# Kernel tuning notes

Measured on AMD Instinct MI355X. Metric: run time of the kernel, lower is better.

## Reference

```python
import jax, jax.numpy as jnp
import numpy as np

H = 51      # lstm_out, hard-coded in the module
L = 3       # num_lstms
IN = 2      # input_dim = f_in(1) + f_time(1)
B = 1024
T = 2048


def _softplus(x):
    # log(1+exp(x)) with the module's inf guard (softplus==inf -> x),
    # written in a grad-safe clipped form (identical in fp32 range).
    x_safe = jnp.minimum(x, 30.0)
    return jnp.where(x > 30.0, x, jnp.log1p(jnp.exp(x_safe)))


def setup_inputs() -> dict:
    key = jax.random.key(0)
    ks = jax.random.split(key, 2 + 4 * L + 2)
    inp = {}
    inp["input"] = jax.random.normal(ks[0], (B, T, 1), dtype=jnp.float32)
    inp["time_idx"] = jax.random.normal(ks[1], (B, T, 1), dtype=jnp.float32)
    k = 1.0 / np.sqrt(H)  # PyTorch LSTMCell/Linear default init scale
    idx = 2
    for l in range(L):
        d_in = IN if l == 0 else H
        inp[f"W_ih{l}"] = jax.random.uniform(ks[idx], (4 * H, d_in), jnp.float32, -k, k); idx += 1
        inp[f"W_hh{l}"] = jax.random.uniform(ks[idx], (4 * H, H), jnp.float32, -k, k); idx += 1
        inp[f"b_ih{l}"] = jax.random.uniform(ks[idx], (4 * H,), jnp.float32, -k, k); idx += 1
        inp[f"b_hh{l}"] = jax.random.uniform(ks[idx], (4 * H,), jnp.float32, -k, k); idx += 1
    inp["W_lin"] = jax.random.uniform(ks[idx], (2, H), jnp.float32, -k, k); idx += 1
    inp["b_lin"] = jax.random.uniform(ks[idx], (2,), jnp.float32, -k, k)
    inp["future"] = 0
    return inp


def _cell(x_t, h, c, W_ih, W_hh, b_ih, b_hh):
    # PyTorch LSTMCell: gates in order i, f, g, o
    gates = x_t @ W_ih.T + b_ih + h @ W_hh.T + b_hh  # (B, 4H)
    i, f, g, o = jnp.split(gates, 4, axis=-1)
    c_new = jax.nn.sigmoid(f) * c + jax.nn.sigmoid(i) * jnp.tanh(g)
    h_new = jax.nn.sigmoid(o) * jnp.tanh(c_new)
    return h_new, c_new


def reference(input, time_idx,
              W_ih0, W_hh0, b_ih0, b_hh0,
              W_ih1, W_hh1, b_ih1, b_hh1,
              W_ih2, W_hh2, b_ih2, b_hh2,
              W_lin, b_lin, future):
    params = [(W_ih0, W_hh0, b_ih0, b_hh0),
              (W_ih1, W_hh1, b_ih1, b_hh1),
              (W_ih2, W_hh2, b_ih2, b_hh2)]
    bsz = input.shape[0]
    # future == 0: time_idx covers exactly the conditioning context
    x = jnp.concatenate([input, time_idx], axis=2)  # (B, T, IN)
    xs = jnp.swapaxes(x, 0, 1)                       # (T, B, IN)
    h0 = jnp.zeros((L, bsz, H), dtype=input.dtype)
    c0 = jnp.zeros((L, bsz, H), dtype=input.dtype)

    def step(carry, x_t):
        hs, cs = carry
        inp_l = x_t
        nh, nc = [], []
        for l, (Wih, Whh, bih, bhh) in enumerate(params):
            h_new, c_new = _cell(inp_l, hs[l], cs[l], Wih, Whh, bih, bhh)
            nh.append(h_new); nc.append(c_new)
            inp_l = h_new
        out = inp_l @ W_lin.T + b_lin  # (B, 2) from linear1
        return (jnp.stack(nh), jnp.stack(nc)), out

    _, outs = jax.lax.scan(step, (h0, c0), xs)  # (T, B, 2)
    outs = jnp.swapaxes(outs, 0, 1)             # (B, T, 2)
    mean = outs[..., 0]
    std = _softplus(outs[..., 1])               # positivity constraint on col 1
    return jnp.stack([mean, std], axis=-1)
```

## Files before the change

kernel.cpp:

```cpp
#include <hip/hip_runtime.h>
#include <cstddef>
#include <cstdint>

#define Hd 51
#define Td 2048
#define NBb 4
#define NTH 768
#define NBLK 256

typedef _Float16 f16x8 __attribute__((ext_vector_type(8)));
typedef _Float16 f16x4 __attribute__((ext_vector_type(4)));
typedef float    f32x4 __attribute__((ext_vector_type(4)));

#define RB0   128
#define RB12  256
#define BASE0 0
#define BASE1 4096
#define BASE2 12288
#define PRE   20480
#define XP    32768
#define LDSB  65536

#define LOG2E  1.44269504f
#define LOG2E2 2.88539008f

__device__ __forceinline__ int vaddr(int base, int rowB, int db, int n, int off) {
    return base + db * (16 * rowB) + ((off >> 4) << 8) + (n << 4) + (off & 15);
}

__device__ __forceinline__ int pslot(int m4, int n) {
    return ((m4 ^ n) & 15) | (n << 4);
}

__device__ __forceinline__ float fast_rcp(float x) { return __builtin_amdgcn_rcpf(x); }
__device__ __forceinline__ float exp2_fast(float x) {
#if __has_builtin(__builtin_amdgcn_exp2f)
    return __builtin_amdgcn_exp2f(x);
#else
    return exp2f(x);
#endif
}

__device__ __forceinline__ float sigm2(float ap)  { return fast_rcp(1.f + exp2_fast(-ap)); }
__device__ __forceinline__ float tanh2(float ap)  { return fmaf(2.f, fast_rcp(1.f + exp2_fast(-ap)), -1.f); }
__device__ __forceinline__ float tanh_c(float x) {
    float e = exp2_fast(-LOG2E2 * fabsf(x));
    float t = (1.f - e) * fast_rcp(1.f + e);
    return copysignf(t, x);
}

__global__ __launch_bounds__(NTH, 3)
void lstm3_mfma(const float* __restrict__ g_input, const float* __restrict__ g_time,
                const float* __restrict__ Wih0, const float* __restrict__ Whh0,
                const float* __restrict__ bih0, const float* __restrict__ bhh0,
                const float* __restrict__ Wih1, const float* __restrict__ Whh1,
                const float* __restrict__ bih1, const float* __restrict__ bhh1,
                const float* __restrict__ Wih2, const float* __restrict__ Whh2,
                const float* __restrict__ bih2, const float* __restrict__ bhh2,
                const float* __restrict__ Wlin, const float* __restrict__ blin,
                float* __restrict__ g_out)
{
    __shared__ __align__(16) unsigned char lds[LDSB];

    const int tid  = threadIdx.x;
    const int lane = tid & 63;
    const int w    = tid >> 6;
    const int g    = w >> 2;
    const int c    = w & 3;
    const int ncol = lane & 15;
    const int kg   = lane >> 4;
    const int b0   = blockIdx.x * NBb;

    for (int i = tid * 4; i < LDSB; i += NTH * 4) *(uint32_t*)(lds + i) = 0u;
    __syncthreads();

    if (tid < 32) {
        int db = tid >> 4, n = tid & 15;
        *(unsigned short*)(lds + vaddr(BASE0, RB0,  db, n,  54 * 2)) = 0x3C00;
        *(unsigned short*)(lds + vaddr(BASE1, RB12, db, n, 112 * 2)) = 0x3C00;
        *(unsigned short*)(lds + vaddr(BASE2, RB12, db, n, 112 * 2)) = 0x3C00;
    } else if (tid >= 64 && tid < 72) {
        int i = tid - 64; int n = i & 3, f = i >> 2;
        const float* src = f ? g_time : g_input;
        float v = src[(size_t)(b0 + n) * Td];
        *(_Float16*)(lds + vaddr(BASE0, RB0, 0, n, (52 + f) * 2)) = (_Float16)v;
    }

    for (int i = tid; i < 4096; i += NTH) {
        const int f  = i >> 11;
        const int rm = i & 2047;
        const int n  = rm >> 9;
        const int t4 = rm & 511;
        const float* src = f ? g_time : g_input;
        float4 v = *(const float4*)&src[(size_t)(b0 + n) * Td + 4 * t4];
        const int slot = f * 4 + n;
        #pragma unroll
        for (int j = 0; j < 4; ++j)
            *(_Float16*)(lds + XP + ((((4 * t4 + j) << 3) + slot) << 1)) = (_Float16)((&v.x)[j]);
    }

    const int er = 16 * c + ncol;
    const bool rvalid = (er < Hd);
    f16x8 AF[16];

    if (g == 0) {
        #pragma unroll
        for (int gs = 0; gs < 4; ++gs) {
            const int sr = gs * Hd + er;
            const float S = (gs == 2) ? LOG2E2 : LOG2E;
            #pragma unroll
            for (int s = 0; s < 2; ++s)
                #pragma unroll
                for (int e = 0; e < 8; ++e) {
                    const int kk = 32 * s + 8 * kg + e;
                    float v = 0.f;
                    if (rvalid) {
                        if (kk < 51)                   v = Whh0[sr * 51 + kk];
                        else if (kk == 52 || kk == 53) v = Wih0[sr * 2 + (kk - 52)];
                        else if (kk == 54)             v = bih0[sr] + bhh0[sr];
                    }
                    AF[gs * 2 + s][e] = (_Float16)(v * S);
                }
        }
    } else {
        const float* Wih = (g == 1) ? Wih1 : Wih2;
        const float* Whh = (g == 1) ? Whh1 : Whh2;
        const float* bihp = (g == 1) ? bih1 : bih2;
        const float* bhhp = (g == 1) ? bhh1 : bhh2;
        #pragma unroll
        for (int gs = 0; gs < 4; ++gs) {
            const int sr = gs * Hd + er;
            const float S = (gs == 2) ? LOG2E2 : LOG2E;
            #pragma unroll
            for (int s = 0; s < 4; ++s)
                #pragma unroll
                for (int e = 0; e < 8; ++e) {
                    const int kk = 32 * s + 8 * kg + e;
                    float v = 0.f;
                    float sc = S;
                    if (rvalid) {
                        if (kk < 51)                   v = Wih[sr * 51 + kk];
                        else if (kk >= 56 && kk < 107) v = Whh[sr * 51 + (kk - 56)];
                        else if (kk == 112)            v = bihp[sr] + bhhp[sr];
                    } else if (g == 2 && gs == 0 && (er == 52 || er == 53)) {
                        const int hr = er - 52;
                        sc = 1.f;
                        if (kk >= 56 && kk < 107)      v = Wlin[hr * 51 + (kk - 56)];
                        else if (kk == 112)            v = blin[hr];
                    }
                    AF[gs * 4 + s][e] = (_Float16)(v * sc);
                }
        }
    }

    const f32x4 Z = {0.f, 0.f, 0.f, 0.f};
    const int PAR0 = 16 * RB0;
    const int PAR12 = 16 * RB12;
    int rd0a = vaddr(BASE0, RB0, 0, ncol, 16 * kg);
    int rd0b = vaddr(BASE0, RB0, 0, ncol, 64 + 16 * kg);
    int rd12[4];
    {
        const int baseg = (g == 2) ? BASE2 : BASE1;
        #pragma unroll
        for (int s = 0; s < 4; ++s) rd12[s] = vaddr(baseg, RB12, 0, ncol, 64 * s + 16 * kg);
    }
    const int e0 = 16 * c + 4 * kg;
    int pw[4];
    bool pwok[4];
    #pragma unroll
    for (int r = 0; r < 4; ++r) {
        pw[r] = PRE + ((g * 4 + c) << 10) + (pslot(4 * kg + r, ncol & 3) << 4);
        pwok[r] = (ncol < 4) && (e0 + r < Hd);
    }

    const bool uok = (lane < 51);
    int prd = 0, wh1 = 0, wh2 = 0, str1 = 0;
    bool has2 = false;
    if (uok) {
        const int u  = w * 51 + lane;
        const int rr = u - g * 204;
        const int ue = rr >> 2;
        const int un = rr & 3;
        prd = PRE + ((g * 4 + (ue >> 4)) << 10) + (pslot(ue & 15, un) << 4);
        if (g == 0) {
            wh1 = vaddr(BASE0, RB0,  0, un, 2 * ue);       str1 = PAR0;
            wh2 = vaddr(BASE1, RB12, 0, un, 2 * ue);       has2 = true;
        } else if (g == 1) {
            wh1 = vaddr(BASE1, RB12, 0, un, 112 + 2 * ue); str1 = PAR12;
            wh2 = vaddr(BASE2, RB12, 0, un, 2 * ue);       has2 = true;
        } else {
            wh1 = vaddr(BASE2, RB12, 0, un, 112 + 2 * ue); str1 = PAR12;
        }
    }
    float ucs = 0.f;

    f16x8 zf;
    #pragma unroll
    for (int e = 0; e < 8; ++e) zf[e] = (_Float16)0.f;
    f16x8 B0 = zf, B1 = zf;
    f16x8 Bv0 = zf, Bv1 = zf, Bv2 = zf, Bv3 = zf;

    __syncthreads();

    for (int n = 0; n <= Td + 2; ++n) {
        const int rb = n & 1, wb = rb ^ 1;
        const int rP0 = rb * PAR0, rP12 = rb * PAR12;

        if (g == 0) {
            const bool dopf = (w == 0 && lane < 8 && (n + 1) < Td);
            _Float16 pfh = (_Float16)0.f;
            const int nb = lane & 3, f = lane >> 2;
            if (dopf)
                pfh = *(const _Float16*)(lds + XP + ((((n + 1) << 3) + lane) << 1));
            if (n < Td) {
                if (ncol < 4) {
                    B0 = *(const f16x8*)(lds + rd0a + rP0);
                    B1 = *(const f16x8*)(lds + rd0b + rP0);
                }
                f32x4 a_i = Z, a_f = Z, a_g = Z, a_o = Z;
                __builtin_amdgcn_s_setprio(1);
                a_i = __builtin_amdgcn_mfma_f32_16x16x32_f16(AF[0], B0, a_i, 0, 0, 0);
                a_i = __builtin_amdgcn_mfma_f32_16x16x32_f16(AF[1], B1, a_i, 0, 0, 0);
                a_f = __builtin_amdgcn_mfma_f32_16x16x32_f16(AF[2], B0, a_f, 0, 0, 0);
                a_f = __builtin_amdgcn_mfma_f32_16x16x32_f16(AF[3], B1, a_f, 0, 0, 0);
                a_g = __builtin_amdgcn_mfma_f32_16x16x32_f16(AF[4], B0, a_g, 0, 0, 0);
                a_g = __builtin_amdgcn_mfma_f32_16x16x32_f16(AF[5], B1, a_g, 0, 0, 0);
                a_o = __builtin_amdgcn_mfma_f32_16x16x32_f16(AF[6], B0, a_o, 0, 0, 0);
                a_o = __builtin_amdgcn_mfma_f32_16x16x32_f16(AF[7], B1, a_o, 0, 0, 0);
                __builtin_amdgcn_s_setprio(0);
                #pragma unroll
                for (int r = 0; r < 4; ++r)
                    if (pwok[r]) {
                        f32x4 v = {a_i[r], a_f[r], a_g[r], a_o[r]};
                        *(f32x4*)(lds + pw[r]) = v;
                    }
            }
            if (dopf)
                *(_Float16*)(lds + vaddr(BASE0, RB0, wb, nb, (52 + f) * 2)) = pfh;
        } else {
            const bool act = (g == 1) ? (n >= 1 && n <= Td) : (n >= 2);
            if (act) {
                if (ncol < 4) {
                    Bv0 = *(const f16x8*)(lds + rd12[0] + rP12);
                    Bv1 = *(const f16x8*)(lds + rd12[1] + rP12);
                    Bv2 = *(const f16x8*)(lds + rd12[2] + rP12);
                    Bv3 = *(const f16x8*)(lds + rd12[3] + rP12);
                }
                f32x4 a_i = Z, a_f = Z, a_g = Z, a_o = Z;
                __builtin_amdgcn_s_setprio(1);
                a_i = __builtin_amdgcn_mfma_f32_16x16x32_f16(AF[0],  Bv0, a_i, 0, 0, 0);
                a_f = __builtin_amdgcn_mfma_f32_16x16x32_f16(AF[4],  Bv0, a_f, 0, 0, 0);
                a_g = __builtin_amdgcn_mfma_f32_16x16x32_f16(AF[8],  Bv0, a_g, 0, 0, 0);
                a_o = __builtin_amdgcn_mfma_f32_16x16x32_f16(AF[12], Bv0, a_o, 0, 0, 0);
                a_i = __builtin_amdgcn_mfma_f32_16x16x32_f16(AF[1],  Bv1, a_i, 0, 0, 0);
                a_f = __builtin_amdgcn_mfma_f32_16x16x32_f16(AF[5],  Bv1, a_f, 0, 0, 0);
                a_g = __builtin_amdgcn_mfma_f32_16x16x32_f16(AF[9],  Bv1, a_g, 0, 0, 0);
                a_o = __builtin_amdgcn_mfma_f32_16x16x32_f16(AF[13], Bv1, a_o, 0, 0, 0);
                a_i = __builtin_amdgcn_mfma_f32_16x16x32_f16(AF[2],  Bv2, a_i, 0, 0, 0);
                a_f = __builtin_amdgcn_mfma_f32_16x16x32_f16(AF[6],  Bv2, a_f, 0, 0, 0);
                a_g = __builtin_amdgcn_mfma_f32_16x16x32_f16(AF[10], Bv2, a_g, 0, 0, 0);
                a_o = __builtin_amdgcn_mfma_f32_16x16x32_f16(AF[14], Bv2, a_o, 0, 0, 0);
                a_i = __builtin_amdgcn_mfma_f32_16x16x32_f16(AF[3],  Bv3, a_i, 0, 0, 0);
                a_f = __builtin_amdgcn_mfma_f32_16x16x32_f16(AF[7],  Bv3, a_f, 0, 0, 0);
                a_g = __builtin_amdgcn_mfma_f32_16x16x32_f16(AF[11], Bv3, a_g, 0, 0, 0);
                a_o = __builtin_amdgcn_mfma_f32_16x16x32_f16(AF[15], Bv3, a_o, 0, 0, 0);
                __builtin_amdgcn_s_setprio(0);
                #pragma unroll
                for (int r = 0; r < 4; ++r)
                    if (pwok[r]) {
                        f32x4 v = {a_i[r], a_f[r], a_g[r], a_o[r]};
                        *(f32x4*)(lds + pw[r]) = v;
                    }
                if (g == 2 && w == 11 && kg == 1 && ncol < 4 && n >= 3) {
                    float mean = a_i[0];
                    float spre = a_i[1];
                    float sp = (spre > 30.f) ? spre : __logf(1.f + __expf(spre));
                    const int t = n - 3;
                    float2 o2 = make_float2(mean, sp);
                    *(float2*)&g_out[((size_t)(b0 + ncol) * Td + t) * 2] = o2;
                }
            }
        }
        __syncthreads();

        if (uok) {
            const int t_u = n - g;
            if (t_u >= 0 && t_u < Td) {
                f32x4 v = *(const f32x4*)(lds + prd);
                float si = sigm2(v[0]);
                float sf = sigm2(v[1]);
                float gg = tanh2(v[2]);
                float go = sigm2(v[3]);
                float cn = fmaf(sf, ucs, si * gg);
                ucs = cn;
                _Float16 hf = (_Float16)(go * tanh_c(cn));
                *(_Float16*)(lds + wh1 + wb * str1) = hf;
                if (has2) *(_Float16*)(lds + wh2 + wb * PAR12) = hf;
            }
        }
        __syncthreads();
    }
}

extern "C" void kernel_launch(void* const* d_in, const int* in_sizes, int n_in,
                              void* d_out, int out_size, void* d_ws, size_t ws_size,
                              hipStream_t stream) {
    const float* input = (const float*)d_in[0];
    const float* timei = (const float*)d_in[1];
    const float* Wih0  = (const float*)d_in[2];
    const float* Whh0  = (const float*)d_in[3];
    const float* bih0  = (const float*)d_in[4];
    const float* bhh0  = (const float*)d_in[5];
    const float* Wih1  = (const float*)d_in[6];
    const float* Whh1  = (const float*)d_in[7];
    const float* bih1  = (const float*)d_in[8];
    const float* bhh1  = (const float*)d_in[9];
    const float* Wih2  = (const float*)d_in[10];
    const float* Whh2  = (const float*)d_in[11];
    const float* bih2  = (const float*)d_in[12];
    const float* bhh2  = (const float*)d_in[13];
    const float* Wlin  = (const float*)d_in[14];
    const float* blin  = (const float*)d_in[15];
    float* out = (float*)d_out;

    lstm3_mfma<<<dim3(NBLK), dim3(NTH), 0, stream>>>(
        input, timei,
        Wih0, Whh0, bih0, bhh0,
        Wih1, Whh1, bih1, bhh1,
        Wih2, Whh2, bih2, bhh2,
        Wlin, blin, out);
}
```

Baseline: 1.985 ms.

## Fuse gate activation into MFMA waves and drop mid-step barrier

Each wave now applies the LSTM cell update to the gate pre-activations it just wrote to LDS, so the update is done by the same wave (mapped by lane to element/batch) instead of a separate pass after a block-wide barrier. This removes one __syncthreads per timestep of the 2051-step recurrence. The output head is also moved into the update path, reading the linear-head results from LDS. It relies on each wave only reading gate values it wrote itself, enforced with an lgkmcnt wait and a scheduling barrier, which is a correctness risk if the slot mapping is wrong.

```diff
diff --git a/kernel.cpp b/kernel.cpp
--- a/kernel.cpp
+++ b/kernel.cpp
@@ -165,32 +165,29 @@
         for (int s = 0; s < 4; ++s) rd12[s] = vaddr(baseg, RB12, 0, ncol, 64 * s + 16 * kg);
     }
     const int e0 = 16 * c + 4 * kg;
+    const int elim = (g == 2) ? 54 : Hd;
     int pw[4];
     bool pwok[4];
     #pragma unroll
     for (int r = 0; r < 4; ++r) {
         pw[r] = PRE + ((g * 4 + c) << 10) + (pslot(4 * kg + r, ncol & 3) << 4);
-        pwok[r] = (ncol < 4) && (e0 + r < Hd);
-    }
-
-    const bool uok = (lane < 51);
-    int prd = 0, wh1 = 0, wh2 = 0, str1 = 0;
-    bool has2 = false;
-    if (uok) {
-        const int u  = w * 51 + lane;
-        const int rr = u - g * 204;
-        const int ue = rr >> 2;
-        const int un = rr & 3;
-        prd = PRE + ((g * 4 + (ue >> 4)) << 10) + (pslot(ue & 15, un) << 4);
-        if (g == 0) {
-            wh1 = vaddr(BASE0, RB0,  0, un, 2 * ue);       str1 = PAR0;
-            wh2 = vaddr(BASE1, RB12, 0, un, 2 * ue);       has2 = true;
-        } else if (g == 1) {
-            wh1 = vaddr(BASE1, RB12, 0, un, 112 + 2 * ue); str1 = PAR12;
-            wh2 = vaddr(BASE2, RB12, 0, un, 2 * ue);       has2 = true;
-        } else {
-            wh1 = vaddr(BASE2, RB12, 0, un, 112 + 2 * ue); str1 = PAR12;
-        }
+        pwok[r] = (ncol < NBb) && (e0 + r < elim);
+    }
+    const int el = lane & 15;
+    const int ub = lane >> 4;
+    const int eg = 16 * c + el;
+    const int prd = PRE + ((g * 4 + c) << 10) + (pslot(el, ub) << 4);
+    const bool upd_ok = (eg < Hd);
+    const bool head_ok = (g == 2 && c == 3 && (el == 4 || el == 5));
+    int wh1, wh2 = -1, str1;
+    if (g == 0) {
+        wh1 = vaddr(BASE0, RB0,  0, ub, 2 * eg);       str1 = PAR0;
+        wh2 = vaddr(BASE1, RB12, 0, ub, 2 * eg);
+    } else if (g == 1) {
+        wh1 = vaddr(BASE1, RB12, 0, ub, 112 + 2 * eg); str1 = PAR12;
+        wh2 = vaddr(BASE2, RB12, 0, ub, 2 * eg);
+    } else {
+        wh1 = vaddr(BASE2, RB12, 0, ub, 112 + 2 * eg); str1 = PAR12;
     }
     float ucs = 0.f;
 
@@ -205,6 +202,7 @@
     for (int n = 0; n <= Td + 2; ++n) {
         const int rb = n & 1, wb = rb ^ 1;
         const int rP0 = rb * PAR0, rP12 = rb * PAR12;
+        const int wP12 = wb * PAR12;
 
         if (g == 0) {
             const bool dopf = (w == 0 && lane < 8 && (n + 1) < Td);
@@ -213,7 +211,7 @@
             if (dopf)
                 pfh = *(const _Float16*)(lds + XP + ((((n + 1) << 3) + lane) << 1));
             if (n < Td) {
-                if (ncol < 4) {
+                if (ncol < NBb) {
                     B0 = *(const f16x8*)(lds + rd0a + rP0);
                     B1 = *(const f16x8*)(lds + rd0b + rP0);
                 }
@@ -234,13 +232,27 @@
                         f32x4 v = {a_i[r], a_f[r], a_g[r], a_o[r]};
                         *(f32x4*)(lds + pw[r]) = v;
                     }
+                asm volatile("s_waitcnt lgkmcnt(0)" ::: "memory");
+                __builtin_amdgcn_sched_barrier(0);
+                f32x4 v = *(const f32x4*)(lds + prd);
+                if (upd_ok) {
+                    float si = sigm2(v[0]);
+                    float sf = sigm2(v[1]);
+                    float gg = tanh2(v[2]);
+                    float go = sigm2(v[3]);
+                    float cn = fmaf(sf, ucs, si * gg);
+                    ucs = cn;
+                    _Float16 hf = (_Float16)(go * tanh_c(cn));
+                    *(_Float16*)(lds + wh1 + wb * str1) = hf;
+                    *(_Float16*)(lds + wh2 + wP12) = hf;
+                }
             }
             if (dopf)
                 *(_Float16*)(lds + vaddr(BASE0, RB0, wb, nb, (52 + f) * 2)) = pfh;
         } else {
             const bool act = (g == 1) ? (n >= 1 && n <= Td) : (n >= 2);
             if (act) {
-                if (ncol < 4) {
+                if (ncol < NBb) {
                     Bv0 = *(const f16x8*)(lds + rd12[0] + rP12);
                     Bv1 = *(const f16x8*)(lds + rd12[1] + rP12);
                     Bv2 = *(const f16x8*)(lds + rd12[2] + rP12);
@@ -271,31 +283,27 @@
                         f32x4 v = {a_i[r], a_f[r], a_g[r], a_o[r]};
                         *(f32x4*)(lds + pw[r]) = v;
                     }
-                if (g == 2 && w == 11 && kg == 1 && ncol < 4 && n >= 3) {
-                    float mean = a_i[0];
-                    float spre = a_i[1];
-                    float sp = (spre > 30.f) ? spre : __logf(1.f + __expf(spre));
+                asm volatile("s_waitcnt lgkmcnt(0)" ::: "memory");
+                __builtin_amdgcn_sched_barrier(0);
+                f32x4 v = *(const f32x4*)(lds + prd);
+                const bool updt = upd_ok && ((g == 1) || (n <= Td + 1));
+                if (updt) {
+                    float si = sigm2(v[0]);
+                    float sf = sigm2(v[1]);
+                    float gg = tanh2(v[2]);
+                    float go = sigm2(v[3]);
+                    float cn = fmaf(sf, ucs, si * gg);
+                    ucs = cn;
+                    _Float16 hf = (_Float16)(go * tanh_c(cn));
+                    *(_Float16*)(lds + wh1 + wb * str1) = hf;
+                    if (g == 1) *(_Float16*)(lds + wh2 + wP12) = hf;
+                }
+                if (head_ok && n >= 3) {
+                    float hv = v[0];
+                    if (el == 5) hv = (hv > 30.f) ? hv : __logf(1.f + __expf(hv));
                     const int t = n - 3;
-                    float2 o2 = make_float2(mean, sp);
-                    *(float2*)&g_out[((size_t)(b0 + ncol) * Td + t) * 2] = o2;
-                }
-            }
-        }
-        __syncthreads();
-
-        if (uok) {
-            const int t_u = n - g;
-            if (t_u >= 0 && t_u < Td) {
-                f32x4 v = *(const f32x4*)(lds + prd);
-                float si = sigm2(v[0]);
-                float sf = sigm2(v[1]);
-                float gg = tanh2(v[2]);
-                float go = sigm2(v[3]);
-                float cn = fmaf(sf, ucs, si * gg);
-                ucs = cn;
-                _Float16 hf = (_Float16)(go * tanh_c(cn));
-                *(_Float16*)(lds + wh1 + wb * str1) = hf;
-                if (has2) *(_Float16*)(lds + wh2 + wb * PAR12) = hf;
+                    g_out[((size_t)(b0 + ub) * Td + t) * 2 + (el - 4)] = hv;
+                }
             }
         }
         __syncthreads();
```

Result: faster. 1.714 ms (-13.6%).
